# Kernel optimization log

Hardware: AMD Instinct MI355X
Metric: run time of the kernel (lower is better)

Reference implementation:

```python
import jax, jax.numpy as jnp
import numpy as np

N = 50000   # num nodes
E = 800000  # num edges (avg degree 16)
D = 128     # in = hidden = out channels


def setup_inputs() -> dict:
    key = jax.random.key(0)
    k0, k1, k2, k3, k4, k5 = jax.random.split(key, 6)
    x = jax.random.normal(k0, (N, D), dtype=jnp.float32)
    edge_index = jax.random.randint(k1, (2, E), 0, N, dtype=jnp.int32)
    scale = 1.0 / np.sqrt(D)
    W1 = jax.random.normal(k2, (D, D), dtype=jnp.float32) * scale
    b1 = jax.random.normal(k3, (D,), dtype=jnp.float32) * 0.01
    W2 = jax.random.normal(k4, (D, D), dtype=jnp.float32) * scale
    b2 = jax.random.normal(k5, (D,), dtype=jnp.float32) * 0.01
    return {"x": x, "edge_index": edge_index, "W1": W1, "b1": b1, "W2": W2, "b2": b2}


def reference(x, edge_index, W1, b1, W2, b2):
    n = x.shape[0]
    src, dst = edge_index[0], edge_index[1]
    # GCN adds self-loops before normalization
    loops = jnp.arange(n, dtype=src.dtype)
    s = jnp.concatenate([src, loops])
    d = jnp.concatenate([dst, loops])
    # symmetric normalization: deg^{-1/2}[s] * deg^{-1/2}[d]
    deg = jax.ops.segment_sum(jnp.ones_like(d, dtype=x.dtype), d, num_segments=n)
    dinv = jnp.where(deg > 0, jax.lax.rsqrt(deg), 0.0)
    ew = dinv[s] * dinv[d]  # [E+N]

    def gcn_conv(h, W, b):
        h = h @ W                                   # [N, D] dense transform first
        msg = ew[:, None] * h[s]                     # gather over edges [E+N, D]
        agg = jax.ops.segment_sum(msg, d, num_segments=n)  # scatter-add [N, D]
        return agg + b

    # layer 1: conv -> Identity BN -> ELU (dropout=0.0 -> no-op)
    h = jax.nn.elu(gcn_conv(x, W1, b1))
    # layer 2 (last): conv -> Identity BN -> ELU
    out = jax.nn.elu(gcn_conv(h, W2, b2))
    return out
```

## Files before the change

kernel.cpp:

```cpp
#include <hip/hip_runtime.h>
#include <math.h>

#define D 128
#define BCAP 8192
#define SLICE 64
#define PB 256

typedef __attribute__((ext_vector_type(8))) short bf16x8;
typedef __attribute__((ext_vector_type(4))) float f32x4;
typedef __attribute__((ext_vector_type(4))) unsigned int u32x4;


__device__ inline float2 bf2f2(unsigned int u) {
    union { unsigned int i; float f; } a, b;
    a.i = u << 16;
    b.i = u & 0xffff0000u;
    return make_float2(a.f, b.f);
}

__device__ inline unsigned short f2bf(float f) {
    union { float f; unsigned int i; } u;
    u.f = f;
    unsigned int r = u.i + 0x7fffu + ((u.i >> 16) & 1u);
    return (unsigned short)(r >> 16);
}

__device__ __forceinline__ float elu_fast(float r) {
    return r > 0.f ? r : __expf(r) - 1.f;
}


__device__ __forceinline__ void gemm_core(unsigned short (*Ws)[136], int gbid,
                                          const void* __restrict__ Ain, int a_fp32,
                                          unsigned int* __restrict__ Cb, int N) {
    const int tid = threadIdx.x;
    const int wid = tid >> 6;
    const int lane = tid & 63;
    const int quad = lane >> 4;
    const int ln = lane & 15;
    const int m = gbid * 64 + wid * 16 + ln;
    const bool valid = (m < N);

    f32x4 acc[8];
#pragma unroll
    for (int c = 0; c < 8; ++c) acc[c] = (f32x4){0.f, 0.f, 0.f, 0.f};

    __syncthreads();

#pragma unroll
    for (int ks = 0; ks < 4; ++ks) {
        const int k0 = ks * 32;
        bf16x8 af;
        if (a_fp32) {
            const float* A = (const float*)Ain;
            float4 lo = make_float4(0.f, 0.f, 0.f, 0.f), hi = lo;
            if (valid) {
                lo = *(const float4*)&A[(size_t)m * 128 + k0 + quad * 8];
                hi = *(const float4*)&A[(size_t)m * 128 + k0 + quad * 8 + 4];
            }
            af[0] = (short)f2bf(lo.x); af[1] = (short)f2bf(lo.y);
            af[2] = (short)f2bf(lo.z); af[3] = (short)f2bf(lo.w);
            af[4] = (short)f2bf(hi.x); af[5] = (short)f2bf(hi.y);
            af[6] = (short)f2bf(hi.z); af[7] = (short)f2bf(hi.w);
        } else {
            const uint4* A4 = (const uint4*)Ain;
            uint4 v = valid ? A4[(size_t)m * 16 + ks * 4 + quad]
                            : make_uint4(0u, 0u, 0u, 0u);
            union { uint4 u; bf16x8 h; } cv;
            cv.u = v;
            af = cv.h;
        }
#pragma unroll
        for (int c = 0; c < 8; ++c) {
            bf16x8 bf = *(const bf16x8*)&Ws[c * 16 + ln][k0 + quad * 8];
            acc[c] = __builtin_amdgcn_mfma_f32_16x16x32_bf16(af, bf, acc[c], 0, 0, 0);
        }
    }

    const int rowbase = gbid * 64 + wid * 16 + quad * 4;
#pragma unroll
    for (int c = 0; c < 8; ++c) {
#pragma unroll
        for (int r = 0; r < 4; ++r) {
            float v = acc[c][r];
            float vn = __shfl_xor(v, 1);
            int grow = rowbase + r;
            if (!(ln & 1) && grow < N) {
                unsigned int u = (unsigned int)f2bf(v) | ((unsigned int)f2bf(vn) << 16);
                Cb[(size_t)grow * 64 + c * 8 + (ln >> 1)] = u;
            }
        }
    }
}


__global__ __launch_bounds__(256) void k1_all(
        const int* __restrict__ src, const int* __restrict__ dst,
        const float* __restrict__ x, const float* __restrict__ W1,
        const float* __restrict__ W2, unsigned short* __restrict__ Wt2,
        unsigned int* __restrict__ pairs, unsigned char* __restrict__ cellCnt,
        unsigned int* __restrict__ hb1, int e, int chunk, int N, int gemmBlocks) {
    __shared__ __align__(16) unsigned char smem[128 * 136 * 2];
    const int tid = threadIdx.x;
    const int bid = blockIdx.x;

    if (bid < PB) {
        int* cur = (int*)smem;
        cur[tid] = 0;
        __syncthreads();
        const int e0 = bid * chunk;
        const int e1 = min(e0 + chunk, e);
        for (int i = e0 + tid; i < e1; i += 256) {
            int d = dst[i], s = src[i];
            int b = d >> 8;
            int off = atomicAdd(&cur[b], 1);
            if (off < SLICE)
                pairs[((size_t)(bid * 256 + b)) * SLICE + off] =
                    (unsigned int)s | ((unsigned int)(d & 255) << 16);
        }
        __syncthreads();
        cellCnt[bid * 256 + tid] = (unsigned char)min(cur[tid], SLICE);
    } else if (bid < PB + gemmBlocks) {
        unsigned short (*Ws)[136] = (unsigned short(*)[136])smem;
        for (int j = 0; j < 64; ++j) {
            int idx = tid + j * 256;
            Ws[idx & 127][idx >> 7] = f2bf(W1[idx]);
        }
        gemm_core(Ws, bid - PB, x, 1, hb1, N);
    } else {
        int i = (bid - PB - gemmBlocks) * 256 + tid;
        int k = i >> 7, n = i & 127;
        Wt2[n * 128 + k] = f2bf(W2[i]);
    }
}


__global__ __launch_bounds__(256) void partB(const unsigned int* __restrict__ pairs,
                                             const unsigned char* __restrict__ cellCnt,
                                             unsigned short* __restrict__ col,
                                             unsigned int* __restrict__ meta,
                                             float* __restrict__ dinv, int n) {
    __shared__ int deg[256];
    __shared__ int sc[256];
    __shared__ int cur[256];
    const int b = blockIdx.x;
    const int tid = threadIdx.x;

    deg[tid] = 0;
    __syncthreads();

    const int c = cellCnt[tid * 256 + b];
    const unsigned int* cell = pairs + ((size_t)(tid * 256 + b)) * SLICE;
    for (int q = 0; q < c; ++q) atomicAdd(&deg[cell[q] >> 16], 1);
    __syncthreads();

    int v = deg[tid];
    sc[tid] = v;
    __syncthreads();
    for (int o = 1; o < 256; o <<= 1) {
        int t = (tid >= o) ? sc[tid - o] : 0;
        __syncthreads();
        sc[tid] += t;
        __syncthreads();
    }
    int startw = sc[tid] - v;
    cur[tid] = startw;

    int node = b * 256 + tid;
    if (node < n) {
        meta[node] = ((unsigned int)(b * BCAP + startw) << 10) | (unsigned int)v;
        dinv[node] = rsqrtf((float)(v + 1));
    }
    __syncthreads();

    for (int q = 0; q < c; ++q) {
        unsigned int p = cell[q];
        int dl = p >> 16;
        int off = atomicAdd(&cur[dl], 1);
        col[(size_t)b * BCAP + off] = (unsigned short)(p & 0xffffu);
    }
}


__device__ __forceinline__ void fma8(float w, u32x4 u, f32x4& a, f32x4& b) {
    float2 v0 = bf2f2(u.x), v1 = bf2f2(u.y), v2 = bf2f2(u.z), v3 = bf2f2(u.w);
    a[0] = fmaf(w, v0.x, a[0]); a[1] = fmaf(w, v0.y, a[1]);
    a[2] = fmaf(w, v1.x, a[2]); a[3] = fmaf(w, v1.y, a[3]);
    b[0] = fmaf(w, v2.x, b[0]); b[1] = fmaf(w, v2.y, b[1]);
    b[2] = fmaf(w, v3.x, b[2]); b[3] = fmaf(w, v3.y, b[3]);
}

__device__ __forceinline__ void add8(u32x4 u, f32x4& a, f32x4& b) {
    float2 v0 = bf2f2(u.x), v1 = bf2f2(u.y), v2 = bf2f2(u.z), v3 = bf2f2(u.w);
    a[0] += v0.x; a[1] += v0.y; a[2] += v1.x; a[3] += v1.y;
    b[0] += v2.x; b[1] += v2.y; b[2] += v3.x; b[3] += v3.y;
}

template <bool PRE>
__device__ __forceinline__ float2 agg_wave_rs(const unsigned int* __restrict__ hb,
                                              const unsigned short* __restrict__ col,
                                              const float* __restrict__ dinv,
                                              int node, int g, int ln,
                                              unsigned int m, float di) {
    const u32x4* hb4 = (const u32x4*)hb;
    const int s0 = (int)(m >> 10);
    const int s1 = s0 + (int)(m & 1023u);

    f32x4 sA = (f32x4){0.f, 0.f, 0.f, 0.f};
    f32x4 sB = (f32x4){0.f, 0.f, 0.f, 0.f};
    {
        u32x4 su = hb4[((unsigned)node << 4) + ln];
        float ws = (g == 0) ? (PRE ? 1.f : di) : 0.f;
        fma8(ws, su, sA, sB);
    }

    int i = s0;
    for (; i + 16 <= s1; i += 16) {
        const int c0 = col[i + g];
        const int c1 = col[i + 4 + g];
        const int c2 = col[i + 8 + g];
        const int c3 = col[i + 12 + g];
        float w0 = 0.f, w1 = 0.f, w2 = 0.f, w3 = 0.f;
        if (!PRE) { w0 = dinv[c0]; w1 = dinv[c1]; w2 = dinv[c2]; w3 = dinv[c3]; }
        u32x4 u0 = hb4[((unsigned)c0 << 4) + ln];
        u32x4 u1 = hb4[((unsigned)c1 << 4) + ln];
        u32x4 u2 = hb4[((unsigned)c2 << 4) + ln];
        u32x4 u3 = hb4[((unsigned)c3 << 4) + ln];
        asm volatile("" :: "v"(u0), "v"(u1), "v"(u2), "v"(u3));
        if (PRE) {
            add8(u0, sA, sB); add8(u1, sA, sB);
            add8(u2, sA, sB); add8(u3, sA, sB);
        } else {
            fma8(w0, u0, sA, sB); fma8(w1, u1, sA, sB);
            fma8(w2, u2, sA, sB); fma8(w3, u3, sA, sB);
        }
    }
    while (i < s1) {
        const int t = i + g;
        const bool ok = (t < s1);
        const int cc = ok ? (int)col[t] : node;
        u32x4 u = hb4[((unsigned)cc << 4) + ln];
        if (PRE) {
            if (ok) add8(u, sA, sB);
        } else {
            const float w = ok ? dinv[cc] : 0.f;
            fma8(w, u, sA, sB);
        }
        i += 4;
    }

    f32x4 t;
#pragma unroll
    for (int k = 0; k < 4; ++k) {
        float pa = __shfl_xor(sA[k], 16);
        float pb = __shfl_xor(sB[k], 16);
        t[k] = (g & 1) ? (sB[k] + pb) : (sA[k] + pa);
    }
    float p0 = __shfl_xor(t[0], 32);
    float p1 = __shfl_xor(t[1], 32);
    float p2 = __shfl_xor(t[2], 32);
    float p3 = __shfl_xor(t[3], 32);
    float e0 = (g & 2) ? (t[2] + p2) : (t[0] + p0);
    float e1 = (g & 2) ? (t[3] + p3) : (t[1] + p1);
    return make_float2(e0, e1);
}


__global__ __launch_bounds__(1024, 4) void k3_agg_gemm(
        const unsigned int* __restrict__ hb1, const unsigned int* __restrict__ meta,
        const unsigned short* __restrict__ col, const float* __restrict__ dinv,
        const float* __restrict__ b1, const unsigned short* __restrict__ Wt2,
        unsigned int* __restrict__ hb2, int n) {
    __shared__ unsigned int g1s[16 * 68];
    __shared__ __align__(16) unsigned short Ws[128][136];

    const int tid = threadIdx.x;
    const int wid = tid >> 6;
    const int lane = tid & 63;
    const int g = lane >> 4;
    const int ln = lane & 15;
    const int nodeBase = blockIdx.x * 16;
    const int node = nodeBase + wid;

    {
        const int nloc = tid >> 3;
        const int kb = (tid & 7) * 16;
        const uint4* gp = (const uint4*)(Wt2 + (size_t)nloc * 128 + kb);
        uint4* sp = (uint4*)&Ws[nloc][kb];
        sp[0] = gp[0];
        sp[1] = gp[1];
    }

    const int cp = 4 * ln + 2 * (g & 1) + (g >> 1);
    if (node < n) {
        const unsigned int m = meta[node];
        const float di = dinv[node];
        float2 e = agg_wave_rs<false>(hb1, col, dinv, node, g, ln, m, di);
        const float2 bv = ((const float2*)b1)[cp];
        float r0 = elu_fast(fmaf(di, e.x, bv.x));
        float r1 = elu_fast(fmaf(di, e.y, bv.y));
        g1s[wid * 68 + cp] = (unsigned int)f2bf(r0) | ((unsigned int)f2bf(r1) << 16);
    } else {
        g1s[wid * 68 + cp] = 0u;
    }
    __syncthreads();

    if (wid < 8) {
        const int quad = lane >> 4;
        f32x4 acc = (f32x4){0.f, 0.f, 0.f, 0.f};
#pragma unroll
        for (int ks = 0; ks < 4; ++ks) {
            bf16x8 af = *(const bf16x8*)&g1s[ln * 68 + ks * 16 + quad * 4];
            bf16x8 bf = *(const bf16x8*)&Ws[wid * 16 + ln][ks * 32 + quad * 8];
            acc = __builtin_amdgcn_mfma_f32_16x16x32_bf16(af, bf, acc, 0, 0, 0);
        }
#pragma unroll
        for (int r = 0; r < 4; ++r) {
            int grow = nodeBase + quad * 4 + r;
            float dsc = (grow < n) ? dinv[grow] : 0.f;
            float v = acc[r] * dsc;
            float vn = __shfl_xor(v, 1);
            if (!(ln & 1) && grow < n) {
                hb2[(size_t)grow * 64 + wid * 8 + (ln >> 1)] =
                    (unsigned int)f2bf(v) | ((unsigned int)f2bf(vn) << 16);
            }
        }
    }
}


__global__ __launch_bounds__(256, 4) void agg_elu(const unsigned int* __restrict__ hb,
                                                  const unsigned int* __restrict__ meta,
                                                  const unsigned short* __restrict__ col,
                                                  const float* __restrict__ dinv,
                                                  const float* __restrict__ bias,
                                                  float* __restrict__ outf, int n) {
    const int wid = threadIdx.x >> 6;
    const int lane = threadIdx.x & 63;
    const int g = lane >> 4;
    const int ln = lane & 15;
    const int node = blockIdx.x * 4 + wid;
    if (node >= n) return;

    const unsigned int m = meta[node];
    const float di = dinv[node];
    float2 e = agg_wave_rs<true>(hb, col, dinv, node, g, ln, m, di);

    const int cp = 4 * ln + 2 * (g & 1) + (g >> 1);
    const float2 bv = ((const float2*)bias)[cp];
    float2 r;
    r.x = elu_fast(fmaf(di, e.x, bv.x));
    r.y = elu_fast(fmaf(di, e.y, bv.y));
    ((float2*)outf)[(size_t)node * 64 + cp] = r;
}


extern "C" void kernel_launch(void* const* d_in, const int* in_sizes, int n_in,
                              void* d_out, int out_size, void* d_ws, size_t ws_size,
                              hipStream_t stream) {
    const float* x  = (const float*)d_in[0];
    const int*   ei = (const int*)d_in[1];
    const float* W1 = (const float*)d_in[2];
    const float* b1 = (const float*)d_in[3];
    const float* W2 = (const float*)d_in[4];
    const float* b2 = (const float*)d_in[5];
    float* out = (float*)d_out;

    const int N = in_sizes[0] / D;
    const int E = in_sizes[1] / 2;
    const int* src = ei;
    const int* dst = ei + E;
    const int NB = (N + 255) / 256;

    char* ws = (char*)d_ws;
    size_t off = 0;
    auto alloc = [&](size_t bytes) -> void* {
        void* p = ws + off;
        off = (off + bytes + 255) & ~(size_t)255;
        return p;
    };
    unsigned int*   pairs   = (unsigned int*)alloc((size_t)PB * 256 * SLICE * 4);
    unsigned char*  cellCnt = (unsigned char*)alloc((size_t)PB * 256);
    unsigned short* col     = (unsigned short*)alloc((size_t)NB * BCAP * 2);
    unsigned int*   meta    = (unsigned int*)alloc((size_t)N * 4);
    float*          dinv    = (float*)alloc((size_t)N * 4);
    unsigned short* Wt2     = (unsigned short*)alloc(128 * 128 * 2);
    unsigned int*   hb1     = (unsigned int*)alloc((size_t)N * 64 * 4);
    unsigned int*   hb2     = (unsigned int*)alloc((size_t)N * 64 * 4);
    (void)ws_size; (void)n_in; (void)out_size;

    const int chunk = (E + PB - 1) / PB;
    const int gemmBlocks = (N + 63) / 64;

    k1_all<<<PB + gemmBlocks + 64, 256, 0, stream>>>(src, dst, x, W1, W2, Wt2,
                                                     pairs, cellCnt, hb1, E, chunk,
                                                     N, gemmBlocks);
    partB<<<NB, 256, 0, stream>>>(pairs, cellCnt, col, meta, dinv, N);
    k3_agg_gemm<<<(N + 15) / 16, 1024, 0, stream>>>(hb1, meta, col, dinv, b1, Wt2, hb2, N);
    agg_elu<<<(N + 3) / 4, 256, 0, stream>>>(hb2, meta, col, dinv, b2, out, N);
}
```

Baseline: 189.2 us.

## Split layer-2 features into channel quarters and widen CSR build blocks

The layer-2 hidden features are now written in four 32-channel planes, each stored contiguously per node. The final aggregation kernel launches one block per node-group and quarter, so each quarter's gather footprint is a quarter the size and can stay in cache. Each 64-byte row is fetched by 16 lanes handling different edges, so one wave covers 16 edges per iteration. Separately, partB uses 1024 threads with four threads per cell, which splits the per-cell atomic loops four ways. The cost is four times as many blocks and four reads of the column indices per node, plus a longer shuffle reduction.

```diff
diff --git a/kernel.cpp b/kernel.cpp
--- a/kernel.cpp
+++ b/kernel.cpp
@@ -135,45 +135,49 @@
 }
 
 
-__global__ __launch_bounds__(256) void partB(const unsigned int* __restrict__ pairs,
-                                             const unsigned char* __restrict__ cellCnt,
-                                             unsigned short* __restrict__ col,
-                                             unsigned int* __restrict__ meta,
-                                             float* __restrict__ dinv, int n) {
+__global__ __launch_bounds__(1024) void partB(const unsigned int* __restrict__ pairs,
+                                              const unsigned char* __restrict__ cellCnt,
+                                              unsigned short* __restrict__ col,
+                                              unsigned int* __restrict__ meta,
+                                              float* __restrict__ dinv, int n) {
     __shared__ int deg[256];
     __shared__ int sc[256];
     __shared__ int cur[256];
     const int b = blockIdx.x;
     const int tid = threadIdx.x;
-
-    deg[tid] = 0;
-    __syncthreads();
-
-    const int c = cellCnt[tid * 256 + b];
-    const unsigned int* cell = pairs + ((size_t)(tid * 256 + b)) * SLICE;
-    for (int q = 0; q < c; ++q) atomicAdd(&deg[cell[q] >> 16], 1);
-    __syncthreads();
-
-    int v = deg[tid];
-    sc[tid] = v;
+    const int ch = tid >> 2;
+    const int sub = tid & 3;
+
+    if (tid < 256) deg[tid] = 0;
+    __syncthreads();
+
+    const int c = min((int)cellCnt[ch * 256 + b], SLICE);
+    const unsigned int* cell = pairs + ((size_t)(ch * 256 + b)) * SLICE;
+    for (int q = sub; q < c; q += 4) atomicAdd(&deg[cell[q] >> 16], 1);
+    __syncthreads();
+
+    if (tid < 256) sc[tid] = deg[tid];
     __syncthreads();
     for (int o = 1; o < 256; o <<= 1) {
-        int t = (tid >= o) ? sc[tid - o] : 0;
+        int t = 0;
+        if (tid < 256 && tid >= o) t = sc[tid - o];
         __syncthreads();
-        sc[tid] += t;
+        if (tid < 256) sc[tid] += t;
         __syncthreads();
     }
-    int startw = sc[tid] - v;
-    cur[tid] = startw;
-
-    int node = b * 256 + tid;
-    if (node < n) {
-        meta[node] = ((unsigned int)(b * BCAP + startw) << 10) | (unsigned int)v;
-        dinv[node] = rsqrtf((float)(v + 1));
-    }
-    __syncthreads();
-
-    for (int q = 0; q < c; ++q) {
+    if (tid < 256) {
+        int v = deg[tid];
+        int startw = sc[tid] - v;
+        cur[tid] = startw;
+        int node = b * 256 + tid;
+        if (node < n) {
+            meta[node] = ((unsigned int)(b * BCAP + startw) << 10) | (unsigned int)v;
+            dinv[node] = rsqrtf((float)(v + 1));
+        }
+    }
+    __syncthreads();
+
+    for (int q = sub; q < c; q += 4) {
         unsigned int p = cell[q];
         int dl = p >> 16;
         int off = atomicAdd(&cur[dl], 1);
@@ -196,7 +200,6 @@
     b[0] += v2.x; b[1] += v2.y; b[2] += v3.x; b[3] += v3.y;
 }
 
-template <bool PRE>
 __device__ __forceinline__ float2 agg_wave_rs(const unsigned int* __restrict__ hb,
                                               const unsigned short* __restrict__ col,
                                               const float* __restrict__ dinv,
@@ -210,7 +213,7 @@
     f32x4 sB = (f32x4){0.f, 0.f, 0.f, 0.f};
     {
         u32x4 su = hb4[((unsigned)node << 4) + ln];
-        float ws = (g == 0) ? (PRE ? 1.f : di) : 0.f;
+        float ws = (g == 0) ? di : 0.f;
         fma8(ws, su, sA, sB);
     }
 
@@ -220,32 +223,22 @@
         const int c1 = col[i + 4 + g];
         const int c2 = col[i + 8 + g];
         const int c3 = col[i + 12 + g];
-        float w0 = 0.f, w1 = 0.f, w2 = 0.f, w3 = 0.f;
-        if (!PRE) { w0 = dinv[c0]; w1 = dinv[c1]; w2 = dinv[c2]; w3 = dinv[c3]; }
+        const float w0 = dinv[c0], w1 = dinv[c1], w2 = dinv[c2], w3 = dinv[c3];
         u32x4 u0 = hb4[((unsigned)c0 << 4) + ln];
         u32x4 u1 = hb4[((unsigned)c1 << 4) + ln];
         u32x4 u2 = hb4[((unsigned)c2 << 4) + ln];
         u32x4 u3 = hb4[((unsigned)c3 << 4) + ln];
         asm volatile("" :: "v"(u0), "v"(u1), "v"(u2), "v"(u3));
-        if (PRE) {
-            add8(u0, sA, sB); add8(u1, sA, sB);
-            add8(u2, sA, sB); add8(u3, sA, sB);
-        } else {
-            fma8(w0, u0, sA, sB); fma8(w1, u1, sA, sB);
-            fma8(w2, u2, sA, sB); fma8(w3, u3, sA, sB);
-        }
+        fma8(w0, u0, sA, sB); fma8(w1, u1, sA, sB);
+        fma8(w2, u2, sA, sB); fma8(w3, u3, sA, sB);
     }
     while (i < s1) {
         const int t = i + g;
         const bool ok = (t < s1);
         const int cc = ok ? (int)col[t] : node;
+        const float w = ok ? dinv[cc] : 0.f;
         u32x4 u = hb4[((unsigned)cc << 4) + ln];
-        if (PRE) {
-            if (ok) add8(u, sA, sB);
-        } else {
-            const float w = ok ? dinv[cc] : 0.f;
-            fma8(w, u, sA, sB);
-        }
+        fma8(w, u, sA, sB);
         i += 4;
     }
 
@@ -295,7 +288,7 @@
     if (node < n) {
         const unsigned int m = meta[node];
         const float di = dinv[node];
-        float2 e = agg_wave_rs<false>(hb1, col, dinv, node, g, ln, m, di);
+        float2 e = agg_wave_rs(hb1, col, dinv, node, g, ln, m, di);
         const float2 bv = ((const float2*)b1)[cp];
         float r0 = elu_fast(fmaf(di, e.x, bv.x));
         float r1 = elu_fast(fmaf(di, e.y, bv.y));
@@ -306,6 +299,7 @@
     __syncthreads();
 
     if (wid < 8) {
+        const size_t qs = (size_t)n * 16;
         const int quad = lane >> 4;
         f32x4 acc = (f32x4){0.f, 0.f, 0.f, 0.f};
 #pragma unroll
@@ -321,7 +315,8 @@
             float v = acc[r] * dsc;
             float vn = __shfl_xor(v, 1);
             if (!(ln & 1) && grow < n) {
-                hb2[(size_t)grow * 64 + wid * 8 + (ln >> 1)] =
+                int p = wid * 8 + (ln >> 1);
+                hb2[(size_t)(p >> 4) * qs + (size_t)grow * 16 + (p & 15)] =
                     (unsigned int)f2bf(v) | ((unsigned int)f2bf(vn) << 16);
             }
         }
@@ -329,29 +324,73 @@
 }
 
 
-__global__ __launch_bounds__(256, 4) void agg_elu(const unsigned int* __restrict__ hb,
-                                                  const unsigned int* __restrict__ meta,
-                                                  const unsigned short* __restrict__ col,
-                                                  const float* __restrict__ dinv,
-                                                  const float* __restrict__ bias,
-                                                  float* __restrict__ outf, int n) {
+__global__ __launch_bounds__(256) void agg2_q(const unsigned int* __restrict__ hb,
+                                              const unsigned int* __restrict__ meta,
+                                              const unsigned short* __restrict__ col,
+                                              const float* __restrict__ dinv,
+                                              const float* __restrict__ bias,
+                                              float* __restrict__ outf, int n) {
+    const int bid = blockIdx.x;
+    const int q = bid & 3;
+    const int k = bid >> 2;
     const int wid = threadIdx.x >> 6;
     const int lane = threadIdx.x & 63;
-    const int g = lane >> 4;
-    const int ln = lane & 15;
-    const int node = blockIdx.x * 4 + wid;
+    const int e = lane & 3;
+    const int j = lane >> 2;
+    const int node = k * 4 + wid;
     if (node >= n) return;
 
     const unsigned int m = meta[node];
     const float di = dinv[node];
-    float2 e = agg_wave_rs<true>(hb, col, dinv, node, g, ln, m, di);
-
-    const int cp = 4 * ln + 2 * (g & 1) + (g >> 1);
-    const float2 bv = ((const float2*)bias)[cp];
-    float2 r;
-    r.x = elu_fast(fmaf(di, e.x, bv.x));
-    r.y = elu_fast(fmaf(di, e.y, bv.y));
-    ((float2*)outf)[(size_t)node * 64 + cp] = r;
+    const int s0 = (int)(m >> 10);
+    const int s1 = s0 + (int)(m & 1023u);
+
+    const u32x4* hq = ((const u32x4*)hb) + (size_t)q * ((size_t)n * 4);
+
+    f32x4 sA = (f32x4){0.f, 0.f, 0.f, 0.f};
+    f32x4 sB = (f32x4){0.f, 0.f, 0.f, 0.f};
+    if (j == 0) {
+        u32x4 su = hq[(size_t)node * 4 + e];
+        add8(su, sA, sB);
+    }
+
+    int i = s0;
+    for (; i + 16 <= s1; i += 16) {
+        int cc = (int)__builtin_nontemporal_load(&col[i + j]);
+        u32x4 u = hq[(size_t)cc * 4 + e];
+        add8(u, sA, sB);
+    }
+    if (i < s1) {
+        if (i + j < s1) {
+            int cc = (int)__builtin_nontemporal_load(&col[i + j]);
+            u32x4 u = hq[(size_t)cc * 4 + e];
+            add8(u, sA, sB);
+        }
+    }
+
+    float t4[4];
+#pragma unroll
+    for (int kk = 0; kk < 4; ++kk) {
+        float pa = __shfl_xor(sA[kk], 4);
+        float pb = __shfl_xor(sB[kk], 4);
+        t4[kk] = (j & 1) ? (sB[kk] + pb) : (sA[kk] + pa);
+    }
+    float t2[2];
+#pragma unroll
+    for (int kk = 0; kk < 2; ++kk) {
+        float p0 = __shfl_xor(t4[kk], 8);
+        float p1 = __shfl_xor(t4[kk + 2], 8);
+        t2[kk] = (j & 2) ? (t4[kk + 2] + p1) : (t4[kk] + p0);
+    }
+    float p0 = __shfl_xor(t2[0], 16);
+    float p1 = __shfl_xor(t2[1], 16);
+    float t1 = (j & 4) ? (t2[1] + p1) : (t2[0] + p0);
+    float t0 = t1 + __shfl_xor(t1, 32);
+
+    const int qc = 8 * e + 4 * (j & 1) + 2 * ((j >> 1) & 1) + ((j >> 2) & 1);
+    const int chg = 32 * q + qc;
+    float r = elu_fast(fmaf(di, t0, bias[chg]));
+    if (j < 8) outf[(size_t)node * 128 + chg] = r;
 }
 
 
@@ -395,7 +434,7 @@
     k1_all<<<PB + gemmBlocks + 64, 256, 0, stream>>>(src, dst, x, W1, W2, Wt2,
                                                      pairs, cellCnt, hb1, E, chunk,
                                                      N, gemmBlocks);
-    partB<<<NB, 256, 0, stream>>>(pairs, cellCnt, col, meta, dinv, N);
+    partB<<<NB, 1024, 0, stream>>>(pairs, cellCnt, col, meta, dinv, N);
     k3_agg_gemm<<<(N + 15) / 16, 1024, 0, stream>>>(hb1, meta, col, dinv, b1, Wt2, hb2, N);
-    agg_elu<<<(N + 3) / 4, 256, 0, stream>>>(hb2, meta, col, dinv, b2, out, N);
-}
+    agg2_q<<<((N + 3) / 4) * 4, 256, 0, stream>>>(hb2, meta, col, dinv, b2, out, N);
+}
```

New measurement: 232.1 us. 22.7% more time.

## Stage partB cells in shared memory and use 1024 threads per block

Applied to the files above, without the earlier changes.

partB now loads every 64-entry cell for its bucket into shared memory with coalesced reads, where before each thread read its own cell serially twice from global memory. The block grows to 1024 threads, and four threads share each cell for both the degree atomics and the scatter. This targets the uncoalesced, latency-bound serial loops. In exchange it uses 64KB of LDS per block, which limits occupancy, and it always loads the full slices even when counts are small.

```diff
diff --git a/kernel.cpp b/kernel.cpp
--- a/kernel.cpp
+++ b/kernel.cpp
@@ -135,46 +135,61 @@
 }
 
 
-__global__ __launch_bounds__(256) void partB(const unsigned int* __restrict__ pairs,
-                                             const unsigned char* __restrict__ cellCnt,
-                                             unsigned short* __restrict__ col,
-                                             unsigned int* __restrict__ meta,
-                                             float* __restrict__ dinv, int n) {
+__global__ __launch_bounds__(1024) void partB(const unsigned int* __restrict__ pairs,
+                                              const unsigned char* __restrict__ cellCnt,
+                                              unsigned short* __restrict__ col,
+                                              unsigned int* __restrict__ meta,
+                                              float* __restrict__ dinv, int n) {
+    __shared__ unsigned int cellS[256][SLICE];
+    __shared__ int cnt[256];
     __shared__ int deg[256];
     __shared__ int sc[256];
     __shared__ int cur[256];
     const int b = blockIdx.x;
     const int tid = threadIdx.x;
-
-    deg[tid] = 0;
-    __syncthreads();
-
-    const int c = cellCnt[tid * 256 + b];
-    const unsigned int* cell = pairs + ((size_t)(tid * 256 + b)) * SLICE;
-    for (int q = 0; q < c; ++q) atomicAdd(&deg[cell[q] >> 16], 1);
-    __syncthreads();
-
-    int v = deg[tid];
-    sc[tid] = v;
+    const int cell0 = tid >> 6;
+    const int slot = tid & 63;
+    const int ch = tid >> 2;
+    const int sub = tid & 3;
+
+#pragma unroll
+    for (int r = 0; r < 16; ++r) {
+        const int cc = r * 16 + cell0;
+        cellS[cc][slot] = pairs[((size_t)(cc * 256 + b)) * SLICE + slot];
+    }
+    if (tid < 256) {
+        cnt[tid] = min((int)cellCnt[tid * 256 + b], SLICE);
+        deg[tid] = 0;
+    }
+    __syncthreads();
+
+    const int c = cnt[ch];
+    for (int q = sub; q < c; q += 4) atomicAdd(&deg[cellS[ch][q] >> 16], 1);
+    __syncthreads();
+
+    if (tid < 256) sc[tid] = deg[tid];
     __syncthreads();
     for (int o = 1; o < 256; o <<= 1) {
-        int t = (tid >= o) ? sc[tid - o] : 0;
+        int t = 0;
+        if (tid < 256 && tid >= o) t = sc[tid - o];
         __syncthreads();
-        sc[tid] += t;
+        if (tid < 256) sc[tid] += t;
         __syncthreads();
     }
-    int startw = sc[tid] - v;
-    cur[tid] = startw;
-
-    int node = b * 256 + tid;
-    if (node < n) {
-        meta[node] = ((unsigned int)(b * BCAP + startw) << 10) | (unsigned int)v;
-        dinv[node] = rsqrtf((float)(v + 1));
-    }
-    __syncthreads();
-
-    for (int q = 0; q < c; ++q) {
-        unsigned int p = cell[q];
+    if (tid < 256) {
+        int v = deg[tid];
+        int startw = sc[tid] - v;
+        cur[tid] = startw;
+        int node = b * 256 + tid;
+        if (node < n) {
+            meta[node] = ((unsigned int)(b * BCAP + startw) << 10) | (unsigned int)v;
+            dinv[node] = rsqrtf((float)(v + 1));
+        }
+    }
+    __syncthreads();
+
+    for (int q = sub; q < c; q += 4) {
+        unsigned int p = cellS[ch][q];
         int dl = p >> 16;
         int off = atomicAdd(&cur[dl], 1);
         col[(size_t)b * BCAP + off] = (unsigned short)(p & 0xffffu);
@@ -395,7 +410,7 @@
     k1_all<<<PB + gemmBlocks + 64, 256, 0, stream>>>(src, dst, x, W1, W2, Wt2,
                                                      pairs, cellCnt, hb1, E, chunk,
                                                      N, gemmBlocks);
-    partB<<<NB, 256, 0, stream>>>(pairs, cellCnt, col, meta, dinv, N);
+    partB<<<NB, 1024, 0, stream>>>(pairs, cellCnt, col, meta, dinv, N);
     k3_agg_gemm<<<(N + 15) / 16, 1024, 0, stream>>>(hb1, meta, col, dinv, b1, Wt2, hb2, N);
     agg_elu<<<(N + 3) / 4, 256, 0, stream>>>(hb2, meta, col, dinv, b2, out, N);
 }
```

Result: no change. 187.0 us (median of 2 runs) (-1.1%).
